# Kernel optimization log

Hardware: AMD Instinct MI355X
Metric: run time of the kernel (lower is better)

The kernel has to match this reference:

```python
import jax, jax.numpy as jnp
import numpy as np

B, L, D_MODEL = 2, 2048, 2048
N_HEADS, N_GROUPS = 16, 4
D_HEAD = D_MODEL // N_HEADS  # 128
H_DIM = 5632
EPS = 1e-6


def rmsnorm(x, g):
    var = jnp.mean(x * x, axis=-1, keepdims=True)
    return x * jax.lax.rsqrt(var + EPS) * g


def apply_rope(x):
    # x: [b, H, l, d_head]; interleaved even/odd rotation as in the source
    l, d_head = x.shape[2], x.shape[3]
    pos = jnp.arange(l, dtype=jnp.float32)[:, None]                      # [l,1]
    div = 10000.0 ** (jnp.arange(0, d_head, 2, dtype=jnp.float32) / d_head)
    cos_e = jnp.cos(pos / div)                                           # [l, d_head//2]
    sin_e = jnp.sin(pos / div)
    xe, xo = x[..., 0::2], x[..., 1::2]
    re = xe * cos_e - xo * sin_e
    ro = xe * sin_e + xo * cos_e
    return jnp.stack([re, ro], axis=-1).reshape(x.shape)


def gqa_attention(q, k, v):
    # q: [b,l,d_model], k/v: [b,l,n_groups*d_head]
    b, l, _ = q.shape
    # faithful to source: direct contiguous view, NO transpose
    q = q.reshape(b, N_HEADS, l, D_HEAD)
    k = k.reshape(b, N_GROUPS, l, D_HEAD)
    v = v.reshape(b, N_GROUPS, l, D_HEAD)
    q = apply_rope(q)
    k = apply_rope(k)
    hpg = N_HEADS // N_GROUPS
    qg = q.reshape(b, N_GROUPS, hpg, l, D_HEAD)
    scale = 1.0 / jnp.sqrt(jnp.asarray(D_HEAD, dtype=q.dtype))
    scores = jnp.einsum('bghqd,bgkd->bghqk', qg, k) * scale              # [b,g,hpg,l,l]
    causal = jnp.tril(jnp.ones((l, l), dtype=bool))
    scores = jnp.where(causal, scores, jnp.asarray(-jnp.inf, scores.dtype))
    p = jax.nn.softmax(scores, axis=-1)
    out = jnp.einsum('bghqk,bgkd->bghqd', p, v)                          # [b,g,hpg,l,d]
    return out.reshape(b, N_HEADS, l, D_HEAD).reshape(b, l, D_MODEL)


def setup_inputs() -> dict:
    key = jax.random.key(0)
    ks = jax.random.split(key, 10)
    s_d = 1.0 / np.sqrt(D_MODEL)
    s_h = 1.0 / np.sqrt(H_DIM)
    return {
        'x': jax.random.normal(ks[0], (B, L, D_MODEL), jnp.float32),
        'g1': jnp.ones((D_MODEL,), jnp.float32),
        'wq': jax.random.normal(ks[1], (D_MODEL, D_MODEL), jnp.float32) * s_d,
        'bq': jnp.zeros((D_MODEL,), jnp.float32),
        'wk': jax.random.normal(ks[2], (D_MODEL, N_GROUPS * D_HEAD), jnp.float32) * s_d,
        'bk': jnp.zeros((N_GROUPS * D_HEAD,), jnp.float32),
        'wv': jax.random.normal(ks[3], (D_MODEL, N_GROUPS * D_HEAD), jnp.float32) * s_d,
        'bv': jnp.zeros((N_GROUPS * D_HEAD,), jnp.float32),
        'wo': jax.random.normal(ks[4], (D_MODEL, D_MODEL), jnp.float32) * s_d,
        'bo': jnp.zeros((D_MODEL,), jnp.float32),
        'g2': jnp.ones((D_MODEL,), jnp.float32),
        'w1': jax.random.normal(ks[5], (D_MODEL, H_DIM), jnp.float32) * s_d,
        'b1': jnp.zeros((H_DIM,), jnp.float32),
        'wg': jax.random.normal(ks[6], (D_MODEL, H_DIM), jnp.float32) * s_d,
        'bg': jnp.zeros((H_DIM,), jnp.float32),
        'w2': jax.random.normal(ks[7], (H_DIM, D_MODEL), jnp.float32) * s_h,
        'b2': jnp.zeros((D_MODEL,), jnp.float32),
    }


def reference(x, g1, wq, bq, wk, bk, wv, bv, wo, bo, g2, w1, b1, wg, bg, w2, b2):
    # pre-norm GQA attention block
    h = rmsnorm(x, g1)
    q = h @ wq + bq
    k = h @ wk + bk
    v = h @ wv + bv
    attn = gqa_attention(q, k, v)
    x = x + attn @ wo + bo
    # pre-norm SwiGLU FFN
    h2 = rmsnorm(x, g2)
    ffn = (jax.nn.silu(h2 @ w1 + b1) * (h2 @ wg + bg)) @ w2 + b2
    return x + ffn
```

## Files before the change

kernel.cpp:

```cpp
#include <hip/hip_runtime.h>
#include <math.h>

#define BATCH 2
#define SEQ 2048
#define DM 2048
#define NH 16
#define NG 4
#define DH 128
#define HDIM 5632
#define MROWS (BATCH * SEQ)
#define KVD (NG * DH)

typedef __attribute__((ext_vector_type(8))) short short8;
typedef __attribute__((ext_vector_type(4))) float f32x4;
typedef unsigned short ushortT;

__device__ __forceinline__ unsigned short f2bf(float x) {
  unsigned int u = __float_as_uint(x);
  u += 0x7FFFu + ((u >> 16) & 1u);
  return (unsigned short)(u >> 16);
}
__device__ __forceinline__ float bf2f(unsigned short h) {
  return __uint_as_float(((unsigned int)h) << 16);
}

__global__ __launch_bounds__(256) void rmsnorm_kernel(
    const float* __restrict__ x, const float* __restrict__ g,
    float* __restrict__ out) {
  int row = blockIdx.x;
  const float4* xr = (const float4*)(x + (size_t)row * DM);
  float4* orow = (float4*)(out + (size_t)row * DM);
  const float4* g4 = (const float4*)g;
  int t = threadIdx.x;
  float4 a = xr[t];
  float4 b = xr[t + 256];
  float ss = a.x * a.x + a.y * a.y + a.z * a.z + a.w * a.w +
             b.x * b.x + b.y * b.y + b.z * b.z + b.w * b.w;
#pragma unroll
  for (int off = 32; off > 0; off >>= 1) ss += __shfl_xor(ss, off);
  __shared__ float red[4];
  if ((t & 63) == 0) red[t >> 6] = ss;
  __syncthreads();
  float tot = red[0] + red[1] + red[2] + red[3];
  float inv = rsqrtf(tot * (1.0f / DM) + 1e-6f);
  float4 ga = g4[t], gb = g4[t + 256];
  float4 oa, ob;
  oa.x = a.x * inv * ga.x; oa.y = a.y * inv * ga.y;
  oa.z = a.z * inv * ga.z; oa.w = a.w * inv * ga.w;
  ob.x = b.x * inv * gb.x; ob.y = b.y * inv * gb.y;
  ob.z = b.z * inv * gb.z; ob.w = b.w * inv * gb.w;
  orow[t] = oa;
  orow[t + 256] = ob;
}

template <int EPI>
__global__ __launch_bounds__(256) void gemm_bf16x3(
    const float* __restrict__ A, const float* __restrict__ W,
    const float* __restrict__ bias, const float* __restrict__ aux,
    float* __restrict__ C, int M, int N, int K) {
  __shared__ unsigned short As[2][128][40];
  __shared__ unsigned short Bs[2][128][40];
  int t = threadIdx.x;
  int lane = t & 63, wid = t >> 6;
  int wr = wid >> 1, wc = wid & 1;
  int row0 = blockIdx.y * 128, col0 = blockIdx.x * 128;

  f32x4 acc[4][4];
#pragma unroll
  for (int mi = 0; mi < 4; mi++)
#pragma unroll
    for (int ni = 0; ni < 4; ni++)
#pragma unroll
      for (int j = 0; j < 4; j++) acc[mi][ni][j] = 0.f;

  int am = t >> 1;
  int ak = (t & 1) * 16;
  int bn = t & 127;
  int bk8 = (t >> 7) * 8;

  int fr = lane & 15, fq = lane >> 4;
  int fk = fq * 8;

  const float* aptr = A + (size_t)(row0 + am) * K + ak;
  const float* wptr = W + (size_t)bk8 * N + col0 + bn;

  float av[16], bv[16];
#pragma unroll
  for (int c = 0; c < 4; c++)
    *(float4*)&av[c * 4] = *(const float4*)&aptr[c * 4];
#pragma unroll
  for (int i = 0; i < 2; i++)
#pragma unroll
    for (int j = 0; j < 8; j++)
      bv[i * 8 + j] = wptr[(size_t)(i * 16 + j) * N];

  for (int k0 = 0; k0 < K; k0 += 32) {
    unsigned short ah[16], al[16], bh[16], bl[16];
#pragma unroll
    for (int e = 0; e < 16; e++) {
      ah[e] = f2bf(av[e]);
      al[e] = f2bf(av[e] - bf2f(ah[e]));
      bh[e] = f2bf(bv[e]);
      bl[e] = f2bf(bv[e] - bf2f(bh[e]));
    }

    __syncthreads();

    *(uint4*)&As[0][am][ak + 0] = *(uint4*)&ah[0];
    *(uint4*)&As[0][am][ak + 8] = *(uint4*)&ah[8];
    *(uint4*)&As[1][am][ak + 0] = *(uint4*)&al[0];
    *(uint4*)&As[1][am][ak + 8] = *(uint4*)&al[8];
#pragma unroll
    for (int i = 0; i < 2; i++) {
      *(uint4*)&Bs[0][bn][bk8 + i * 16] = *(uint4*)&bh[i * 8];
      *(uint4*)&Bs[1][bn][bk8 + i * 16] = *(uint4*)&bl[i * 8];
    }

    __syncthreads();

    if (k0 + 32 < K) {
      const float* ap = aptr + (k0 + 32);
      const float* wp = wptr + (size_t)(k0 + 32) * N;
#pragma unroll
      for (int c = 0; c < 4; c++)
        *(float4*)&av[c * 4] = *(const float4*)&ap[c * 4];
#pragma unroll
      for (int i = 0; i < 2; i++)
#pragma unroll
        for (int j = 0; j < 8; j++)
          bv[i * 8 + j] = wp[(size_t)(i * 16 + j) * N];
    }

    short8 bfr[4][2];
#pragma unroll
    for (int ni = 0; ni < 4; ni++) {
      int brow = wc * 64 + ni * 16 + fr;
      bfr[ni][0] = *(const short8*)&Bs[0][brow][fk];
      bfr[ni][1] = *(const short8*)&Bs[1][brow][fk];
    }
#pragma unroll
    for (int mi = 0; mi < 4; mi++) {
      int arow = wr * 64 + mi * 16 + fr;
      short8 a_h = *(const short8*)&As[0][arow][fk];
      short8 a_l = *(const short8*)&As[1][arow][fk];
#pragma unroll
      for (int ni = 0; ni < 4; ni++) {
        acc[mi][ni] = __builtin_amdgcn_mfma_f32_16x16x32_bf16(
            a_h, bfr[ni][0], acc[mi][ni], 0, 0, 0);
        acc[mi][ni] = __builtin_amdgcn_mfma_f32_16x16x32_bf16(
            a_h, bfr[ni][1], acc[mi][ni], 0, 0, 0);
        acc[mi][ni] = __builtin_amdgcn_mfma_f32_16x16x32_bf16(
            a_l, bfr[ni][0], acc[mi][ni], 0, 0, 0);
      }
    }
  }

#pragma unroll
  for (int mi = 0; mi < 4; mi++) {
#pragma unroll
    for (int ni = 0; ni < 4; ni++) {
      int row = row0 + wr * 64 + mi * 16 + fq * 4;
      int col = col0 + wc * 64 + ni * 16 + fr;
      float bc = bias[col];
#pragma unroll
      for (int j = 0; j < 4; j++) {
        size_t idx = (size_t)(row + j) * N + col;
        float v = acc[mi][ni][j] + bc;
        if (EPI == 1) v += aux[idx];
        if (EPI == 2) {
          float u = aux[idx];
          v = (u / (1.f + expf(-u))) * v;
        }
        C[idx] = v;
      }
    }
  }
}

__global__ __launch_bounds__(256) void rope_table_kernel(float* __restrict__ tab) {
  int idx = blockIdx.x * 256 + threadIdx.x;
  if (idx >= SEQ * 64) return;
  int l = idx >> 6, i = idx & 63;
  double div = pow(10000.0, (double)(2 * i) / (double)DH);
  double ang = (double)l / div;
  tab[idx * 2 + 0] = (float)cos(ang);
  tab[idx * 2 + 1] = (float)sin(ang);
}

__global__ __launch_bounds__(256) void gather_rope_q_bf(
    const float* __restrict__ qmat, const float* __restrict__ tab,
    ushortT* __restrict__ Qh, ushortT* __restrict__ Ql) {
  int gid = blockIdx.x * 4 + (threadIdx.x >> 6);
  int lane = threadIdx.x & 63;
  int b = gid >> 15;
  int rem = gid & 32767;
  int h = rem >> 11, l2 = rem & 2047;
  int srow = h * 128 + (l2 >> 4);
  int scol = (l2 & 15) * 128;
  const float2* src = (const float2*)(qmat + ((size_t)b * SEQ + srow) * DM + scol);
  float2 v = src[lane];
  float2 cs = ((const float2*)tab)[l2 * 64 + lane];
  const float scale = 0.08838834764831845f;
  float ox = (v.x * cs.x - v.y * cs.y) * scale;
  float oy = (v.x * cs.y + v.y * cs.x) * scale;
  ushortT hx = f2bf(ox), hy = f2bf(oy);
  ushortT lx = f2bf(ox - bf2f(hx)), ly = f2bf(oy - bf2f(hy));
  size_t o = (size_t)gid * DH + 2 * lane;
  Qh[o] = hx; Qh[o + 1] = hy;
  Ql[o] = lx; Ql[o + 1] = ly;
}

__global__ __launch_bounds__(256) void gather_k_bf(
    const float* __restrict__ mat, const float* __restrict__ tab,
    ushortT* __restrict__ Kh, ushortT* __restrict__ Kl) {
  int gid = blockIdx.x * 4 + (threadIdx.x >> 6);
  int lane = threadIdx.x & 63;
  int b = gid >> 13;
  int rem = gid & 8191;
  int g = rem >> 11, l2 = rem & 2047;
  int srow = g * 512 + (l2 >> 2);
  int scol = (l2 & 3) * 128;
  const float2* src = (const float2*)(mat + ((size_t)b * SEQ + srow) * KVD + scol);
  float2 v = src[lane];
  float2 cs = ((const float2*)tab)[l2 * 64 + lane];
  float ox = v.x * cs.x - v.y * cs.y;
  float oy = v.x * cs.y + v.y * cs.x;
  ushortT hx = f2bf(ox), hy = f2bf(oy);
  ushortT lx = f2bf(ox - bf2f(hx)), ly = f2bf(oy - bf2f(hy));
  size_t o = (size_t)gid * DH + 2 * lane;
  Kh[o] = hx; Kh[o + 1] = hy;
  Kl[o] = lx; Kl[o + 1] = ly;
}

__global__ __launch_bounds__(256) void gather_vt_bf(
    const float* __restrict__ vmat, ushortT* __restrict__ Vth,
    ushortT* __restrict__ Vtl) {
  __shared__ float Ls[64][33];
  int t = threadIdx.x;
  int bg = blockIdx.z;
  int b = bg >> 2, g = bg & 3;
  int l2base = blockIdx.x * 64, dbase = blockIdx.y * 32;

  int l2 = l2base + (t >> 2);
  int srow = g * 512 + (l2 >> 2);
  int scol = (l2 & 3) * 128 + dbase + (t & 3) * 8;
  const float* src = vmat + ((size_t)b * SEQ + srow) * KVD + scol;
  float4 v0 = *(const float4*)src;
  float4 v1 = *(const float4*)(src + 4);
  int lr = t >> 2, lc = (t & 3) * 8;
  Ls[lr][lc + 0] = v0.x; Ls[lr][lc + 1] = v0.y;
  Ls[lr][lc + 2] = v0.z; Ls[lr][lc + 3] = v0.w;
  Ls[lr][lc + 4] = v1.x; Ls[lr][lc + 5] = v1.y;
  Ls[lr][lc + 6] = v1.z; Ls[lr][lc + 7] = v1.w;
  __syncthreads();
  short8 hv, lv;
#pragma unroll
  for (int i = 0; i < 8; i++) {
    float v = Ls[(t & 7) * 8 + i][t >> 3];
    unsigned short h = f2bf(v);
    hv[i] = (short)h;
    lv[i] = (short)f2bf(v - bf2f(h));
  }
  size_t o = ((size_t)bg * DH + dbase + (t >> 3)) * SEQ + l2base + (t & 7) * 8;
  *(short8*)(Vth + o) = hv;
  *(short8*)(Vtl + o) = lv;
}

__global__ __launch_bounds__(256) void attn_mfma(
    const ushortT* __restrict__ Qh, const ushortT* __restrict__ Ql,
    const ushortT* __restrict__ Kh, const ushortT* __restrict__ Kl,
    const ushortT* __restrict__ Vth, const ushortT* __restrict__ Vtl,
    float* __restrict__ O) {
  __shared__ ushortT Ks[2][32][136];
  __shared__ ushortT Vts[2][128][40];
  __shared__ ushortT Ps[4][2][16][40];
  int t = threadIdx.x;
  int lane = t & 63, w = t >> 6;
  int fr = lane & 15, fq = lane >> 4;
  int bh = blockIdx.y;
  int bg = (bh >> 4) * NG + ((bh & 15) >> 2);
  int q0 = ((int)gridDim.x - 1 - (int)blockIdx.x) * 64;

  short8 qfh[4], qfl[4];
  {
    const ushortT* qs = Qh + ((size_t)bh * SEQ + q0 + w * 16 + fr) * DH + fq * 8;
    const ushortT* qs2 = Ql + ((size_t)bh * SEQ + q0 + w * 16 + fr) * DH + fq * 8;
#pragma unroll
    for (int ks = 0; ks < 4; ks++) {
      qfh[ks] = *(const short8*)(qs + ks * 32);
      qfl[ks] = *(const short8*)(qs2 + ks * 32);
    }
  }

  f32x4 oacc[8];
#pragma unroll
  for (int nt = 0; nt < 8; nt++)
#pragma unroll
    for (int j = 0; j < 4; j++) oacc[nt][j] = 0.f;
  float m[4], l[4];
#pragma unroll
  for (int j = 0; j < 4; j++) { m[j] = -INFINITY; l[j] = 0.f; }

  int nkt = q0 / 32 + 2;
  for (int kt = 0; kt < nkt; kt++) {
    int p = t >> 7, tt = t & 127;
    int kr = tt >> 2, cb = (tt & 3) * 32;
    const ushortT* ksp =
        (p ? Kl : Kh) + ((size_t)bg * SEQ + kt * 32 + kr) * DH + cb;
    uint4 k0 = *(const uint4*)(ksp + 0), k1 = *(const uint4*)(ksp + 8);
    uint4 k2 = *(const uint4*)(ksp + 16), k3 = *(const uint4*)(ksp + 24);
    const ushortT* vsp = (p ? Vtl : Vth) + ((size_t)bg * DH + tt) * SEQ + kt * 32;
    uint4 v0 = *(const uint4*)(vsp + 0), v1 = *(const uint4*)(vsp + 8);
    uint4 v2 = *(const uint4*)(vsp + 16), v3 = *(const uint4*)(vsp + 24);

    __syncthreads();
    *(uint4*)&Ks[p][kr][cb + 0] = k0;
    *(uint4*)&Ks[p][kr][cb + 8] = k1;
    *(uint4*)&Ks[p][kr][cb + 16] = k2;
    *(uint4*)&Ks[p][kr][cb + 24] = k3;
    int xs = (tt & 3) << 3;
    *(uint4*)&Vts[p][tt][0 ^ xs] = v0;
    *(uint4*)&Vts[p][tt][8 ^ xs] = v1;
    *(uint4*)&Vts[p][tt][16 ^ xs] = v2;
    *(uint4*)&Vts[p][tt][24 ^ xs] = v3;
    __syncthreads();

    f32x4 sc[2];
#pragma unroll
    for (int ct = 0; ct < 2; ct++)
#pragma unroll
      for (int j = 0; j < 4; j++) sc[ct][j] = 0.f;
#pragma unroll
    for (int ct = 0; ct < 2; ct++)
#pragma unroll
      for (int ks = 0; ks < 4; ks++) {
        short8 kfh = *(const short8*)&Ks[0][ct * 16 + fr][ks * 32 + fq * 8];
        short8 kfl = *(const short8*)&Ks[1][ct * 16 + fr][ks * 32 + fq * 8];
        sc[ct] = __builtin_amdgcn_mfma_f32_16x16x32_bf16(qfh[ks], kfh, sc[ct], 0, 0, 0);
        sc[ct] = __builtin_amdgcn_mfma_f32_16x16x32_bf16(qfh[ks], kfl, sc[ct], 0, 0, 0);
        sc[ct] = __builtin_amdgcn_mfma_f32_16x16x32_bf16(qfl[ks], kfh, sc[ct], 0, 0, 0);
      }

    float alpha[4];
#pragma unroll
    for (int j = 0; j < 4; j++) {
      int qg = q0 + w * 16 + fq * 4 + j;
      float s0 = (kt * 32 + fr <= qg) ? sc[0][j] : -INFINITY;
      float s1 = (kt * 32 + 16 + fr <= qg) ? sc[1][j] : -INFINITY;
      float mx = fmaxf(s0, s1);
      mx = fmaxf(mx, __shfl_xor(mx, 1));
      mx = fmaxf(mx, __shfl_xor(mx, 2));
      mx = fmaxf(mx, __shfl_xor(mx, 4));
      mx = fmaxf(mx, __shfl_xor(mx, 8));
      float mn = fmaxf(m[j], mx);
      float al = expf(m[j] - mn);
      float p0 = expf(s0 - mn), p1 = expf(s1 - mn);
      float rs = p0 + p1;
      rs += __shfl_xor(rs, 1);
      rs += __shfl_xor(rs, 2);
      rs += __shfl_xor(rs, 4);
      rs += __shfl_xor(rs, 8);
      l[j] = l[j] * al + rs;
      m[j] = mn;
      alpha[j] = al;
      ushortT p0h = f2bf(p0), p1h = f2bf(p1);
      Ps[w][0][fq * 4 + j][fr] = p0h;
      Ps[w][0][fq * 4 + j][16 + fr] = p1h;
      Ps[w][1][fq * 4 + j][fr] = f2bf(p0 - bf2f(p0h));
      Ps[w][1][fq * 4 + j][16 + fr] = f2bf(p1 - bf2f(p1h));
    }
#pragma unroll
    for (int nt = 0; nt < 8; nt++) {
      oacc[nt][0] *= alpha[0];
      oacc[nt][1] *= alpha[1];
      oacc[nt][2] *= alpha[2];
      oacc[nt][3] *= alpha[3];
    }

    short8 pah = *(const short8*)&Ps[w][0][fr][fq * 8];
    short8 pal = *(const short8*)&Ps[w][1][fr][fq * 8];
#pragma unroll
    for (int nt = 0; nt < 8; nt++) {
      int vr = nt * 16 + fr;
      int vc = (fq * 8) ^ ((fr & 3) << 3);
      short8 vfh = *(const short8*)&Vts[0][vr][vc];
      short8 vfl = *(const short8*)&Vts[1][vr][vc];
      oacc[nt] = __builtin_amdgcn_mfma_f32_16x16x32_bf16(pah, vfh, oacc[nt], 0, 0, 0);
      oacc[nt] = __builtin_amdgcn_mfma_f32_16x16x32_bf16(pah, vfl, oacc[nt], 0, 0, 0);
      oacc[nt] = __builtin_amdgcn_mfma_f32_16x16x32_bf16(pal, vfh, oacc[nt], 0, 0, 0);
    }
  }

  float inv[4];
#pragma unroll
  for (int j = 0; j < 4; j++) inv[j] = 1.f / l[j];
  float* ob = O + ((size_t)bh * SEQ + q0 + w * 16 + fq * 4) * DH + fr;
#pragma unroll
  for (int nt = 0; nt < 8; nt++)
#pragma unroll
    for (int j = 0; j < 4; j++)
      ob[(size_t)j * DH + nt * 16] = oacc[nt][j] * inv[j];
}

__global__ __launch_bounds__(256) void scatter_o(const float* __restrict__ O,
                                                 float* __restrict__ attn) {
  size_t i4 = (size_t)blockIdx.x * 256 + threadIdx.x;
  size_t f = i4 * 4;
  int b = (int)(f >> 22);
  int rem = (int)(f & 4194303);
  int l = rem >> 11, d = rem & 2047;
  int c = l * 16 + (d >> 7);
  int h = c >> 11, l2 = c & 2047, d2 = d & 127;
  float4 v = *(const float4*)&O[(((size_t)b * NH + h) * SEQ + l2) * DH + d2];
  *(float4*)&attn[f] = v;
}

extern "C" void kernel_launch(void* const* d_in, const int* in_sizes, int n_in,
                              void* d_out, int out_size, void* d_ws,
                              size_t ws_size, hipStream_t stream) {
  if (ws_size < 48496640ull * 4ull) return;

  const float* x  = (const float*)d_in[0];
  const float* g1 = (const float*)d_in[1];
  const float* wq = (const float*)d_in[2];
  const float* bq = (const float*)d_in[3];
  const float* wk = (const float*)d_in[4];
  const float* bk = (const float*)d_in[5];
  const float* wv = (const float*)d_in[6];
  const float* bv = (const float*)d_in[7];
  const float* wo = (const float*)d_in[8];
  const float* bo = (const float*)d_in[9];
  const float* g2 = (const float*)d_in[10];
  const float* w1 = (const float*)d_in[11];
  const float* b1 = (const float*)d_in[12];
  const float* wg = (const float*)d_in[13];
  const float* bg = (const float*)d_in[14];
  const float* w2 = (const float*)d_in[15];
  const float* b2 = (const float*)d_in[16];
  float* out = (float*)d_out;
  float* ws = (float*)d_ws;

  float* buf_h  = ws + 0;
  float* buf_q  = ws + 8388608;
  float* buf_k  = ws + 16777216;
  float* buf_v  = ws + 18874368;
  float* buf_x2 = ws + 16777216;
  ushortT* Qh  = (ushortT*)(ws + 25165824);
  ushortT* Ql  = (ushortT*)(ws + 29360128);
  ushortT* Kh  = (ushortT*)(ws + 33554432);
  ushortT* Kl  = (ushortT*)(ws + 34603008);
  ushortT* Vth = (ushortT*)(ws + 35651584);
  ushortT* Vtl = (ushortT*)(ws + 36700160);
  float* buf_u = ws + 25165824;
  float* tab   = ws + 48234496;

  rope_table_kernel<<<(SEQ * 64 + 255) / 256, 256, 0, stream>>>(tab);
  rmsnorm_kernel<<<MROWS, 256, 0, stream>>>(x, g1, buf_h);

  gemm_bf16x3<0><<<dim3(DM / 128, MROWS / 128), 256, 0, stream>>>(
      buf_h, wq, bq, nullptr, buf_q, MROWS, DM, DM);
  gemm_bf16x3<0><<<dim3(KVD / 128, MROWS / 128), 256, 0, stream>>>(
      buf_h, wk, bk, nullptr, buf_k, MROWS, KVD, DM);
  gemm_bf16x3<0><<<dim3(KVD / 128, MROWS / 128), 256, 0, stream>>>(
      buf_h, wv, bv, nullptr, buf_v, MROWS, KVD, DM);

  gather_rope_q_bf<<<(BATCH * NH * SEQ) / 4, 256, 0, stream>>>(buf_q, tab, Qh, Ql);
  gather_k_bf<<<(BATCH * NG * SEQ) / 4, 256, 0, stream>>>(buf_k, tab, Kh, Kl);
  gather_vt_bf<<<dim3(SEQ / 64, DH / 32, BATCH * NG), 256, 0, stream>>>(
      buf_v, Vth, Vtl);

  attn_mfma<<<dim3(SEQ / 64, BATCH * NH), 256, 0, stream>>>(
      Qh, Ql, Kh, Kl, Vth, Vtl, buf_h);
  scatter_o<<<(MROWS * DM / 4) / 256, 256, 0, stream>>>(buf_h, buf_q);

  gemm_bf16x3<1><<<dim3(DM / 128, MROWS / 128), 256, 0, stream>>>(
      buf_q, wo, bo, x, buf_x2, MROWS, DM, DM);

  rmsnorm_kernel<<<MROWS, 256, 0, stream>>>(buf_x2, g2, buf_h);

  gemm_bf16x3<0><<<dim3(HDIM / 128, MROWS / 128), 256, 0, stream>>>(
      buf_h, w1, b1, nullptr, buf_u, MROWS, HDIM, DM);
  gemm_bf16x3<2><<<dim3(HDIM / 128, MROWS / 128), 256, 0, stream>>>(
      buf_h, wg, bg, buf_u, buf_u, MROWS, HDIM, DM);

  gemm_bf16x3<1><<<dim3(DM / 128, MROWS / 128), 256, 0, stream>>>(
      buf_u, w2, b2, buf_x2, out, MROWS, DM, HDIM);
}
```

Before: 2.215 ms.

## Pre-split activations and weights into bf16 hi/lo planes before GEMMs

New measurement: 2.026 ms. -8.6%, faster.

```diff
diff --git a/kernel.cpp b/kernel.cpp
--- a/kernel.cpp
+++ b/kernel.cpp
@@ -13,6 +13,7 @@
 
 typedef __attribute__((ext_vector_type(8))) short short8;
 typedef __attribute__((ext_vector_type(4))) float f32x4;
+typedef __attribute__((ext_vector_type(4))) unsigned short us4;
 typedef unsigned short ushortT;
 
 __device__ __forceinline__ unsigned short f2bf(float x) {
@@ -24,12 +25,11 @@
   return __uint_as_float(((unsigned int)h) << 16);
 }
 
-__global__ __launch_bounds__(256) void rmsnorm_kernel(
+__global__ __launch_bounds__(256) void rmsnorm_planes(
     const float* __restrict__ x, const float* __restrict__ g,
-    float* __restrict__ out) {
+    ushortT* __restrict__ Ah, ushortT* __restrict__ Al) {
   int row = blockIdx.x;
   const float4* xr = (const float4*)(x + (size_t)row * DM);
-  float4* orow = (float4*)(out + (size_t)row * DM);
   const float4* g4 = (const float4*)g;
   int t = threadIdx.x;
   float4 a = xr[t];
@@ -44,22 +44,64 @@
   float tot = red[0] + red[1] + red[2] + red[3];
   float inv = rsqrtf(tot * (1.0f / DM) + 1e-6f);
   float4 ga = g4[t], gb = g4[t + 256];
-  float4 oa, ob;
-  oa.x = a.x * inv * ga.x; oa.y = a.y * inv * ga.y;
-  oa.z = a.z * inv * ga.z; oa.w = a.w * inv * ga.w;
-  ob.x = b.x * inv * gb.x; ob.y = b.y * inv * gb.y;
-  ob.z = b.z * inv * gb.z; ob.w = b.w * inv * gb.w;
-  orow[t] = oa;
-  orow[t + 256] = ob;
+  float va[4] = {a.x * inv * ga.x, a.y * inv * ga.y, a.z * inv * ga.z,
+                 a.w * inv * ga.w};
+  float vb[4] = {b.x * inv * gb.x, b.y * inv * gb.y, b.z * inv * gb.z,
+                 b.w * inv * gb.w};
+  us4 ha, la, hb, lb;
+#pragma unroll
+  for (int i = 0; i < 4; i++) {
+    ushortT h = f2bf(va[i]);
+    ha[i] = h; la[i] = f2bf(va[i] - bf2f(h));
+    h = f2bf(vb[i]);
+    hb[i] = h; lb[i] = f2bf(vb[i] - bf2f(h));
+  }
+  size_t o = (size_t)row * DM + 4 * t;
+  *(us4*)&Ah[o] = ha; *(us4*)&Al[o] = la;
+  *(us4*)&Ah[o + 1024] = hb; *(us4*)&Al[o + 1024] = lb;
+}
+
+__global__ __launch_bounds__(256) void split_wt(
+    const float* __restrict__ W, ushortT* __restrict__ Wth,
+    ushortT* __restrict__ Wtl, int K, int N) {
+  __shared__ float Ls[64][65];
+  int t = threadIdx.x;
+  int nb = blockIdx.x * 64, kb = blockIdx.y * 64;
+  int lr = t >> 4, lc = (t & 15) * 4;
+#pragma unroll
+  for (int r = 0; r < 4; r++) {
+    float4 v = *(const float4*)&W[(size_t)(kb + lr + r * 16) * N + nb + lc];
+    Ls[lr + r * 16][lc + 0] = v.x;
+    Ls[lr + r * 16][lc + 1] = v.y;
+    Ls[lr + r * 16][lc + 2] = v.z;
+    Ls[lr + r * 16][lc + 3] = v.w;
+  }
+  __syncthreads();
+  int nr = t >> 2, kc = (t & 3) * 16;
+  ushortT hv[16], lv[16];
+#pragma unroll
+  for (int i = 0; i < 16; i++) {
+    float v = Ls[kc + i][nr];
+    hv[i] = f2bf(v);
+    lv[i] = f2bf(v - bf2f(hv[i]));
+  }
+  size_t o = (size_t)(nb + nr) * K + kb + kc;
+  *(uint4*)&Wth[o] = *(uint4*)&hv[0];
+  *(uint4*)&Wth[o + 8] = *(uint4*)&hv[8];
+  *(uint4*)&Wtl[o] = *(uint4*)&lv[0];
+  *(uint4*)&Wtl[o + 8] = *(uint4*)&lv[8];
 }
 
 template <int EPI>
-__global__ __launch_bounds__(256) void gemm_bf16x3(
-    const float* __restrict__ A, const float* __restrict__ W,
-    const float* __restrict__ bias, const float* __restrict__ aux,
-    float* __restrict__ C, int M, int N, int K) {
-  __shared__ unsigned short As[2][128][40];
-  __shared__ unsigned short Bs[2][128][40];
+__global__ __launch_bounds__(256) void gemm_pl(
+    const ushortT* __restrict__ Ah, const ushortT* __restrict__ Al,
+    const ushortT* __restrict__ Wth, const ushortT* __restrict__ Wtl,
+    const float* __restrict__ bias, const float* __restrict__ auxf,
+    const ushortT* __restrict__ auxh, const ushortT* __restrict__ auxl,
+    float* __restrict__ Cf, ushortT* __restrict__ Ch,
+    ushortT* __restrict__ Cl, int M, int N, int K) {
+  __shared__ ushortT As[2][128][40];
+  __shared__ ushortT Bs[2][128][40];
   int t = threadIdx.x;
   int lane = t & 63, wid = t >> 6;
   int wr = wid >> 1, wc = wid & 1;
@@ -73,62 +115,42 @@
 #pragma unroll
       for (int j = 0; j < 4; j++) acc[mi][ni][j] = 0.f;
 
-  int am = t >> 1;
-  int ak = (t & 1) * 16;
-  int bn = t & 127;
-  int bk8 = (t >> 7) * 8;
-
+  int am = t >> 1, ak = (t & 1) * 16;
+  int bn = t & 127, bk = (t >> 7) * 16;
   int fr = lane & 15, fq = lane >> 4;
   int fk = fq * 8;
 
-  const float* aptr = A + (size_t)(row0 + am) * K + ak;
-  const float* wptr = W + (size_t)bk8 * N + col0 + bn;
-
-  float av[16], bv[16];
-#pragma unroll
-  for (int c = 0; c < 4; c++)
-    *(float4*)&av[c * 4] = *(const float4*)&aptr[c * 4];
-#pragma unroll
-  for (int i = 0; i < 2; i++)
-#pragma unroll
-    for (int j = 0; j < 8; j++)
-      bv[i * 8 + j] = wptr[(size_t)(i * 16 + j) * N];
+  const ushortT* a0 = Ah + (size_t)(row0 + am) * K + ak;
+  const ushortT* a1 = Al + (size_t)(row0 + am) * K + ak;
+  const ushortT* b0 = Wth + (size_t)(col0 + bn) * K + bk;
+  const ushortT* b1 = Wtl + (size_t)(col0 + bn) * K + bk;
+
+  uint4 ra0 = *(const uint4*)(a0), ra1 = *(const uint4*)(a0 + 8);
+  uint4 ra2 = *(const uint4*)(a1), ra3 = *(const uint4*)(a1 + 8);
+  uint4 rb0 = *(const uint4*)(b0), rb1 = *(const uint4*)(b0 + 8);
+  uint4 rb2 = *(const uint4*)(b1), rb3 = *(const uint4*)(b1 + 8);
 
   for (int k0 = 0; k0 < K; k0 += 32) {
-    unsigned short ah[16], al[16], bh[16], bl[16];
-#pragma unroll
-    for (int e = 0; e < 16; e++) {
-      ah[e] = f2bf(av[e]);
-      al[e] = f2bf(av[e] - bf2f(ah[e]));
-      bh[e] = f2bf(bv[e]);
-      bl[e] = f2bf(bv[e] - bf2f(bh[e]));
-    }
-
     __syncthreads();
-
-    *(uint4*)&As[0][am][ak + 0] = *(uint4*)&ah[0];
-    *(uint4*)&As[0][am][ak + 8] = *(uint4*)&ah[8];
-    *(uint4*)&As[1][am][ak + 0] = *(uint4*)&al[0];
-    *(uint4*)&As[1][am][ak + 8] = *(uint4*)&al[8];
-#pragma unroll
-    for (int i = 0; i < 2; i++) {
-      *(uint4*)&Bs[0][bn][bk8 + i * 16] = *(uint4*)&bh[i * 8];
-      *(uint4*)&Bs[1][bn][bk8 + i * 16] = *(uint4*)&bl[i * 8];
-    }
-
+    *(uint4*)&As[0][am][ak + 0] = ra0;
+    *(uint4*)&As[0][am][ak + 8] = ra1;
+    *(uint4*)&As[1][am][ak + 0] = ra2;
+    *(uint4*)&As[1][am][ak + 8] = ra3;
+    *(uint4*)&Bs[0][bn][bk + 0] = rb0;
+    *(uint4*)&Bs[0][bn][bk + 8] = rb1;
+    *(uint4*)&Bs[1][bn][bk + 0] = rb2;
+    *(uint4*)&Bs[1][bn][bk + 8] = rb3;
     __syncthreads();
 
     if (k0 + 32 < K) {
-      const float* ap = aptr + (k0 + 32);
-      const float* wp = wptr + (size_t)(k0 + 32) * N;
-#pragma unroll
-      for (int c = 0; c < 4; c++)
-        *(float4*)&av[c * 4] = *(const float4*)&ap[c * 4];
-#pragma unroll
-      for (int i = 0; i < 2; i++)
-#pragma unroll
-        for (int j = 0; j < 8; j++)
-          bv[i * 8 + j] = wp[(size_t)(i * 16 + j) * N];
+      ra0 = *(const uint4*)(a0 + k0 + 32);
+      ra1 = *(const uint4*)(a0 + k0 + 40);
+      ra2 = *(const uint4*)(a1 + k0 + 32);
+      ra3 = *(const uint4*)(a1 + k0 + 40);
+      rb0 = *(const uint4*)(b0 + k0 + 32);
+      rb1 = *(const uint4*)(b0 + k0 + 40);
+      rb2 = *(const uint4*)(b1 + k0 + 32);
+      rb3 = *(const uint4*)(b1 + k0 + 40);
     }
 
     short8 bfr[4][2];
@@ -166,12 +188,18 @@
       for (int j = 0; j < 4; j++) {
         size_t idx = (size_t)(row + j) * N + col;
         float v = acc[mi][ni][j] + bc;
-        if (EPI == 1) v += aux[idx];
-        if (EPI == 2) {
-          float u = aux[idx];
-          v = (u / (1.f + expf(-u))) * v;
+        if (EPI == 1) v += auxf[idx];
+        if (EPI == 3) {
+          float u = bf2f(auxh[idx]) + bf2f(auxl[idx]);
+          v = v * (u / (1.f + expf(-u)));
         }
-        C[idx] = v;
+        if (EPI <= 1) {
+          Cf[idx] = v;
+        } else {
+          ushortT h = f2bf(v);
+          Ch[idx] = h;
+          Cl[idx] = f2bf(v - bf2f(h));
+        }
       }
     }
   }
@@ -200,7 +228,7 @@
   const float2* src = (const float2*)(qmat + ((size_t)b * SEQ + srow) * DM + scol);
   float2 v = src[lane];
   float2 cs = ((const float2*)tab)[l2 * 64 + lane];
-  const float scale = 0.08838834764831845f;
+  const float scale = (float)(0.08838834764831845 * 1.4426950408889634);
   float ox = (v.x * cs.x - v.y * cs.y) * scale;
   float oy = (v.x * cs.y + v.y * cs.x) * scale;
   ushortT hx = f2bf(ox), hy = f2bf(oy);
@@ -240,7 +268,6 @@
   int bg = blockIdx.z;
   int b = bg >> 2, g = bg & 3;
   int l2base = blockIdx.x * 64, dbase = blockIdx.y * 32;
-
   int l2 = l2base + (t >> 2);
   int srow = g * 512 + (l2 >> 2);
   int scol = (l2 & 3) * 128 + dbase + (t & 3) * 8;
@@ -273,7 +300,7 @@
     float* __restrict__ O) {
   __shared__ ushortT Ks[2][32][136];
   __shared__ ushortT Vts[2][128][40];
-  __shared__ ushortT Ps[4][2][16][40];
+  __shared__ ushortT Ps[4][16][40];
   int t = threadIdx.x;
   int lane = t & 63, w = t >> 6;
   int fr = lane & 15, fq = lane >> 4;
@@ -353,8 +380,8 @@
       mx = fmaxf(mx, __shfl_xor(mx, 4));
       mx = fmaxf(mx, __shfl_xor(mx, 8));
       float mn = fmaxf(m[j], mx);
-      float al = expf(m[j] - mn);
-      float p0 = expf(s0 - mn), p1 = expf(s1 - mn);
+      float al = exp2f(m[j] - mn);
+      float p0 = exp2f(s0 - mn), p1 = exp2f(s1 - mn);
       float rs = p0 + p1;
       rs += __shfl_xor(rs, 1);
       rs += __shfl_xor(rs, 2);
@@ -363,11 +390,8 @@
       l[j] = l[j] * al + rs;
       m[j] = mn;
       alpha[j] = al;
-      ushortT p0h = f2bf(p0), p1h = f2bf(p1);
-      Ps[w][0][fq * 4 + j][fr] = p0h;
-      Ps[w][0][fq * 4 + j][16 + fr] = p1h;
-      Ps[w][1][fq * 4 + j][fr] = f2bf(p0 - bf2f(p0h));
-      Ps[w][1][fq * 4 + j][16 + fr] = f2bf(p1 - bf2f(p1h));
+      Ps[w][fq * 4 + j][fr] = f2bf(p0);
+      Ps[w][fq * 4 + j][16 + fr] = f2bf(p1);
     }
 #pragma unroll
     for (int nt = 0; nt < 8; nt++) {
@@ -377,8 +401,7 @@
       oacc[nt][3] *= alpha[3];
     }
 
-    short8 pah = *(const short8*)&Ps[w][0][fr][fq * 8];
-    short8 pal = *(const short8*)&Ps[w][1][fr][fq * 8];
+    short8 pah = *(const short8*)&Ps[w][fr][fq * 8];
 #pragma unroll
     for (int nt = 0; nt < 8; nt++) {
       int vr = nt * 16 + fr;
@@ -387,7 +410,6 @@
       short8 vfl = *(const short8*)&Vts[1][vr][vc];
       oacc[nt] = __builtin_amdgcn_mfma_f32_16x16x32_bf16(pah, vfh, oacc[nt], 0, 0, 0);
       oacc[nt] = __builtin_amdgcn_mfma_f32_16x16x32_bf16(pah, vfl, oacc[nt], 0, 0, 0);
-      oacc[nt] = __builtin_amdgcn_mfma_f32_16x16x32_bf16(pal, vfh, oacc[nt], 0, 0, 0);
     }
   }
 
@@ -402,8 +424,9 @@
       ob[(size_t)j * DH + nt * 16] = oacc[nt][j] * inv[j];
 }
 
-__global__ __launch_bounds__(256) void scatter_o(const float* __restrict__ O,
-                                                 float* __restrict__ attn) {
+__global__ __launch_bounds__(256) void scatter_o_planes(
+    const float* __restrict__ O, ushortT* __restrict__ Sh,
+    ushortT* __restrict__ Sl) {
   size_t i4 = (size_t)blockIdx.x * 256 + threadIdx.x;
   size_t f = i4 * 4;
   int b = (int)(f >> 22);
@@ -412,13 +435,22 @@
   int c = l * 16 + (d >> 7);
   int h = c >> 11, l2 = c & 2047, d2 = d & 127;
   float4 v = *(const float4*)&O[(((size_t)b * NH + h) * SEQ + l2) * DH + d2];
-  *(float4*)&attn[f] = v;
+  float vv[4] = {v.x, v.y, v.z, v.w};
+  us4 hv, lv;
+#pragma unroll
+  for (int i = 0; i < 4; i++) {
+    ushortT h16 = f2bf(vv[i]);
+    hv[i] = h16;
+    lv[i] = f2bf(vv[i] - bf2f(h16));
+  }
+  *(us4*)&Sh[f] = hv;
+  *(us4*)&Sl[f] = lv;
 }
 
 extern "C" void kernel_launch(void* const* d_in, const int* in_sizes, int n_in,
                               void* d_out, int out_size, void* d_ws,
                               size_t ws_size, hipStream_t stream) {
-  if (ws_size < 48496640ull * 4ull) return;
+  if (ws_size < 53739520ull * 4ull) return;
 
   const float* x  = (const float*)d_in[0];
   const float* g1 = (const float*)d_in[1];
@@ -440,49 +472,68 @@
   float* out = (float*)d_out;
   float* ws = (float*)d_ws;
 
-  float* buf_h  = ws + 0;
-  float* buf_q  = ws + 8388608;
-  float* buf_k  = ws + 16777216;
-  float* buf_v  = ws + 18874368;
-  float* buf_x2 = ws + 16777216;
-  ushortT* Qh  = (ushortT*)(ws + 25165824);
-  ushortT* Ql  = (ushortT*)(ws + 29360128);
-  ushortT* Kh  = (ushortT*)(ws + 33554432);
-  ushortT* Kl  = (ushortT*)(ws + 34603008);
-  ushortT* Vth = (ushortT*)(ws + 35651584);
-  ushortT* Vtl = (ushortT*)(ws + 36700160);
-  float* buf_u = ws + 25165824;
-  float* tab   = ws + 48234496;
+  ushortT* WTh = (ushortT*)(ws + 0);
+  ushortT* Hh  = (ushortT*)(ws + 11534336);
+  ushortT* Hl  = Hh + 8388608;
+  float* qmat  = ws + 19922944;
+  float* kmat  = ws + 28311552;
+  float* vmat  = ws + 30408704;
+  ushortT* Qh  = (ushortT*)(ws + 32505856);
+  ushortT* Ql  = Qh + 8388608;
+  ushortT* Kh  = (ushortT*)(ws + 40894464);
+  ushortT* Kl  = Kh + 2097152;
+  ushortT* Vth = (ushortT*)(ws + 42991616);
+  ushortT* Vtl = Vth + 2097152;
+  float* x2    = ws + 45088768;
+  float* tab   = ws + 53477376;
+  float* O     = qmat;
+  ushortT* Sh  = Qh;
+  ushortT* Sl  = Sh + 8388608;
+  ushortT* Uh  = (ushortT*)qmat;
+  ushortT* Ul  = Uh + 23068672;
 
   rope_table_kernel<<<(SEQ * 64 + 255) / 256, 256, 0, stream>>>(tab);
-  rmsnorm_kernel<<<MROWS, 256, 0, stream>>>(x, g1, buf_h);
-
-  gemm_bf16x3<0><<<dim3(DM / 128, MROWS / 128), 256, 0, stream>>>(
-      buf_h, wq, bq, nullptr, buf_q, MROWS, DM, DM);
-  gemm_bf16x3<0><<<dim3(KVD / 128, MROWS / 128), 256, 0, stream>>>(
-      buf_h, wk, bk, nullptr, buf_k, MROWS, KVD, DM);
-  gemm_bf16x3<0><<<dim3(KVD / 128, MROWS / 128), 256, 0, stream>>>(
-      buf_h, wv, bv, nullptr, buf_v, MROWS, KVD, DM);
-
-  gather_rope_q_bf<<<(BATCH * NH * SEQ) / 4, 256, 0, stream>>>(buf_q, tab, Qh, Ql);
-  gather_k_bf<<<(BATCH * NG * SEQ) / 4, 256, 0, stream>>>(buf_k, tab, Kh, Kl);
-  gather_vt_bf<<<dim3(SEQ / 64, DH / 32, BATCH * NG), 256, 0, stream>>>(
-      buf_v, Vth, Vtl);
-
-  attn_mfma<<<dim3(SEQ / 64, BATCH * NH), 256, 0, stream>>>(
-      Qh, Ql, Kh, Kl, Vth, Vtl, buf_h);
-  scatter_o<<<(MROWS * DM / 4) / 256, 256, 0, stream>>>(buf_h, buf_q);
-
-  gemm_bf16x3<1><<<dim3(DM / 128, MROWS / 128), 256, 0, stream>>>(
-      buf_q, wo, bo, x, buf_x2, MROWS, DM, DM);
-
-  rmsnorm_kernel<<<MROWS, 256, 0, stream>>>(buf_x2, g2, buf_h);
-
-  gemm_bf16x3<0><<<dim3(HDIM / 128, MROWS / 128), 256, 0, stream>>>(
-      buf_h, w1, b1, nullptr, buf_u, MROWS, HDIM, DM);
-  gemm_bf16x3<2><<<dim3(HDIM / 128, MROWS / 128), 256, 0, stream>>>(
-      buf_h, wg, bg, buf_u, buf_u, MROWS, HDIM, DM);
-
-  gemm_bf16x3<1><<<dim3(DM / 128, MROWS / 128), 256, 0, stream>>>(
-      buf_u, w2, b2, buf_x2, out, MROWS, DM, HDIM);
-}
+  rmsnorm_planes<<<MROWS, 256, 0, stream>>>(x, g1, Hh, Hl);
+
+  split_wt<<<dim3(DM / 64, DM / 64), 256, 0, stream>>>(wq, WTh, WTh + DM * DM, DM, DM);
+  gemm_pl<0><<<dim3(DM / 128, MROWS / 128), 256, 0, stream>>>(
+      Hh, Hl, WTh, WTh + DM * DM, bq, nullptr, nullptr, nullptr, qmat, nullptr,
+      nullptr, MROWS, DM, DM);
+  split_wt<<<dim3(KVD / 64, DM / 64), 256, 0, stream>>>(wk, WTh, WTh + DM * KVD, DM, KVD);
+  gemm_pl<0><<<dim3(KVD / 128, MROWS / 128), 256, 0, stream>>>(
+      Hh, Hl, WTh, WTh + DM * KVD, bk, nullptr, nullptr, nullptr, kmat, nullptr,
+      nullptr, MROWS, KVD, DM);
+  split_wt<<<dim3(KVD / 64, DM / 64), 256, 0, stream>>>(wv, WTh, WTh + DM * KVD, DM, KVD);
+  gemm_pl<0><<<dim3(KVD / 128, MROWS / 128), 256, 0, stream>>>(
+      Hh, Hl, WTh, WTh + DM * KVD, bv, nullptr, nullptr, nullptr, vmat, nullptr,
+      nullptr, MROWS, KVD, DM);
+
+  gather_rope_q_bf<<<(BATCH * NH * SEQ) / 4, 256, 0, stream>>>(qmat, tab, Qh, Ql);
+  gather_k_bf<<<(BATCH * NG * SEQ) / 4, 256, 0, stream>>>(kmat, tab, Kh, Kl);
+  gather_vt_bf<<<dim3(SEQ / 64, DH / 32, BATCH * NG), 256, 0, stream>>>(vmat, Vth, Vtl);
+
+  attn_mfma<<<dim3(SEQ / 64, BATCH * NH), 256, 0, stream>>>(Qh, Ql, Kh, Kl,
+                                                            Vth, Vtl, O);
+  scatter_o_planes<<<(MROWS * DM / 4) / 256, 256, 0, stream>>>(O, Sh, Sl);
+
+  split_wt<<<dim3(DM / 64, DM / 64), 256, 0, stream>>>(wo, WTh, WTh + DM * DM, DM, DM);
+  gemm_pl<1><<<dim3(DM / 128, MROWS / 128), 256, 0, stream>>>(
+      Sh, Sl, WTh, WTh + DM * DM, bo, x, nullptr, nullptr, x2, nullptr,
+      nullptr, MROWS, DM, DM);
+
+  rmsnorm_planes<<<MROWS, 256, 0, stream>>>(x2, g2, Hh, Hl);
+
+  split_wt<<<dim3(HDIM / 64, DM / 64), 256, 0, stream>>>(w1, WTh, WTh + DM * HDIM, DM, HDIM);
+  gemm_pl<2><<<dim3(HDIM / 128, MROWS / 128), 256, 0, stream>>>(
+      Hh, Hl, WTh, WTh + DM * HDIM, b1, nullptr, nullptr, nullptr, nullptr, Uh,
+      Ul, MROWS, HDIM, DM);
+  split_wt<<<dim3(HDIM / 64, DM / 64), 256, 0, stream>>>(wg, WTh, WTh + DM * HDIM, DM, HDIM);
+  gemm_pl<3><<<dim3(HDIM / 128, MROWS / 128), 256, 0, stream>>>(
+      Hh, Hl, WTh, WTh + DM * HDIM, bg, nullptr, Uh, Ul, nullptr, Uh, Ul,
+      MROWS, HDIM, DM);
+
+  split_wt<<<dim3(DM / 64, HDIM / 64), 256, 0, stream>>>(w2, WTh, WTh + HDIM * DM, HDIM, DM);
+  gemm_pl<1><<<dim3(DM / 128, MROWS / 128), 256, 0, stream>>>(
+      Uh, Ul, WTh, WTh + HDIM * DM, b2, x2, nullptr, nullptr, out, nullptr,
+      nullptr, MROWS, DM, HDIM);
+}
```
